# Optimization experiments

Hardware: AMD Instinct MI355X
Metric: run time of the kernel (lower is better)

Reference implementation:

```python
import jax, jax.numpy as jnp
import numpy as np

B, N, F_IN, F_OUT = 16, 1024, 128, 128
LEAKY_SLOPE = 0.01  # torch nn.LeakyReLU default


def setup_inputs() -> dict:
    key = jax.random.key(0)
    k1, k2, k3, k4 = jax.random.split(key, 4)
    node_mat = jax.random.normal(k1, (B, N, F_IN), dtype=jnp.float32)
    adj_mat = jax.random.uniform(k2, (B, N, N), dtype=jnp.float32)
    # nn.Linear(node_in_len, node_out_len): weight [F_OUT, F_IN], bias [F_OUT]
    bound = 1.0 / np.sqrt(F_IN)
    W = jax.random.uniform(k3, (F_OUT, F_IN), minval=-bound, maxval=bound, dtype=jnp.float32)
    b = jax.random.uniform(k4, (F_OUT,), minval=-bound, maxval=bound, dtype=jnp.float32)
    return {"node_mat": node_mat, "adj_mat": adj_mat, "W": W, "b": b}


def reference(node_mat, adj_mat, W, b):
    # degree normalization: row-scale adjacency by 1/degree
    # (the torch code builds a diagonal inv-degree matrix and bmm's it;
    #  mathematically identical to a broadcast row scale)
    n_neighbors = adj_mat.sum(axis=-1, keepdims=True)          # [B, N, 1]
    norm_adj = adj_mat / n_neighbors                           # [B, N, N]
    node_fea = jnp.einsum('bnm,bmf->bnf', norm_adj, node_mat)  # [B, N, F_in]
    node_fea = jnp.einsum('bnf,of->bno', node_fea, W) + b      # linear
    return jnp.where(node_fea >= 0, node_fea, LEAKY_SLOPE * node_fea)
```

## Files before the change

### kernel.cpp

```cpp
#include <hip/hip_runtime.h>
#include <hip/hip_bf16.h>


typedef __attribute__((ext_vector_type(8))) __bf16 bf16x8;
typedef __attribute__((ext_vector_type(4))) float f32x4;

#define GLD16(gp, lp) __builtin_amdgcn_global_load_lds( \
    (const __attribute__((address_space(1))) unsigned int*)(gp), \
    (__attribute__((address_space(3))) unsigned int*)(lp), 16, 0, 0)

#define WAITV8()  do { asm volatile("s_waitcnt vmcnt(8)" ::: "memory"); \
                       __builtin_amdgcn_sched_barrier(0); } while (0)
#define WAITV0()  do { asm volatile("s_waitcnt vmcnt(0)" ::: "memory"); \
                       __builtin_amdgcn_sched_barrier(0); } while (0)
#define BARF()    do { __builtin_amdgcn_s_barrier(); \
                       __builtin_amdgcn_sched_barrier(0); } while (0)

__device__ __forceinline__ unsigned f2bf_pk(float lo, float hi) {
    union { float f; unsigned u; } a, b;
    a.f = lo; b.f = hi;
    unsigned ra = (a.u + 0x7FFFu + ((a.u >> 16) & 1u)) >> 16;
    unsigned rb = (b.u + 0x7FFFu + ((b.u >> 16) & 1u)) & 0xFFFF0000u;
    return ra | rb;
}

__device__ __forceinline__ bf16x8 cvt8(const f32x4& a, const f32x4& b) {
    union { unsigned u[4]; bf16x8 v; } r;
    r.u[0] = f2bf_pk(a.x, a.y);
    r.u[1] = f2bf_pk(a.z, a.w);
    r.u[2] = f2bf_pk(b.x, b.y);
    r.u[3] = f2bf_pk(b.z, b.w);
    return r.v;
}

__global__ __launch_bounds__(256, 4)
void k1_xw(const float* __restrict__ x, const float* __restrict__ W,
           unsigned short* __restrict__ yF)
{
    __shared__ unsigned short Ax[16 * 128];
    __shared__ unsigned short Bw[128 * 128];

    const int t  = threadIdx.x;
    const int wg = blockIdx.x;
    const int b  = wg >> 6;
    const int m0 = (wg & 63) << 4;
    const float* xb = x + (((long)b << 10) + m0) * 128;

#pragma unroll
    for (int i = 0; i < 2; ++i) {
        int e = i * 1024 + t * 4;
        int r = e >> 7, f = e & 127;
        f32x4 v = *(const f32x4*)(xb + (long)r * 128 + f);
        int c = f >> 3;
        int byte = r * 256 + (((c ^ (r & 7)) << 4) | ((f & 7) << 1));
        uint2 pk; pk.x = f2bf_pk(v.x, v.y); pk.y = f2bf_pk(v.z, v.w);
        *(uint2*)((char*)Ax + byte) = pk;
    }
#pragma unroll
    for (int i = 0; i < 16; ++i) {
        int e = i * 1024 + t * 4;
        int r = e >> 7, f = e & 127;
        f32x4 v = *(const f32x4*)(W + r * 128 + f);
        int c = f >> 3;
        int byte = r * 256 + (((c ^ (r & 7)) << 4) | ((f & 7) << 1));
        uint2 pk; pk.x = f2bf_pk(v.x, v.y); pk.y = f2bf_pk(v.z, v.w);
        *(uint2*)((char*)Bw + byte) = pk;
    }
    __syncthreads();

    const int lane = t & 63, w = t >> 6;
    const int lrow = lane & 15, lq = lane >> 4;

    bf16x8 af[4];
#pragma unroll
    for (int kk = 0; kk < 4; ++kk) {
        int r = lrow;
        int c = kk * 4 + lq;
        af[kk] = *(const bf16x8*)((const char*)Ax + r * 256 + ((c ^ (r & 7)) << 4));
    }

    f32x4 zero = {0.f, 0.f, 0.f, 0.f};
    f32x4 acc[2] = {zero, zero};
#pragma unroll
    for (int nf = 0; nf < 2; ++nf) {
#pragma unroll
        for (int kk = 0; kk < 4; ++kk) {
            int o = (w * 2 + nf) * 16 + lrow;
            int c = kk * 4 + lq;
            bf16x8 bfrag = *(const bf16x8*)((const char*)Bw + o * 256 + ((c ^ (o & 7)) << 4));
            acc[nf] = __builtin_amdgcn_mfma_f32_16x16x32_bf16(af[kk], bfrag, acc[nf], 0, 0, 0);
        }
    }

    {
        const int ks = m0 >> 5;
        const int q  = ((m0 >> 4) & 1) * 2 + (lq >> 1);
        const int jb = (lq & 1) * 4;
#pragma unroll
        for (int nf = 0; nf < 2; ++nf) {
            int ot = w * 2 + nf;
            uint2 pk;
            pk.x = f2bf_pk(acc[nf][0], acc[nf][1]);
            pk.y = f2bf_pk(acc[nf][2], acc[nf][3]);
            long off = (((long)((b * 32 + ks) * 8 + ot)) << 9) + (q * 16 + lrow) * 8 + jb;
            *(uint2*)(yF + off) = pk;
        }
    }
}

__global__ __launch_bounds__(512, 1)
void k2_agg(const float* __restrict__ adj, const unsigned short* __restrict__ yF,
            const float* __restrict__ bias, float* __restrict__ out)
{
    __shared__ float          bufA[2][64 * 128];
    __shared__ unsigned short bufY[2][32 * 512];

    const int bid = blockIdx.x;
    const int xcd = bid & 7;
    const int j   = bid >> 3;
    const int b   = xcd * 2 + (j >> 4);
    const int n0  = (j & 15) << 6;

    const int t = threadIdx.x;
    const int lane = t & 63, w = t >> 6;
    const int h = w >> 1, oc = w & 1;
    const int lrow = lane & 15, lq = lane >> 4;

    const float* adjb = adj + ((long)b << 20);
    const int srow = (lane >> 5);
    const int ssc  = lane & 31;

    const float* ag[4];
    int adst[4];
#pragma unroll
    for (int i = 0; i < 4; ++i) {
        int rl = w * 8 + 2 * i + srow;
        ag[i]   = adjb + ((long)(n0 + rl) << 10) + ((ssc ^ (rl & 7)) << 2);
        adst[i] = (w * 8 + 2 * i) * 128;
    }
    const unsigned short* yg[4];
    int ydst[4];
#pragma unroll
    for (int i = 0; i < 4; ++i) {
        int f = w * 4 + i;
        yg[i]   = yF + (((long)((b * 32 + (f >> 3)) * 8 + (f & 7))) << 9) + lane * 8;
        ydst[i] = f << 9;
    }

    f32x4 zero = {0.f, 0.f, 0.f, 0.f};
    f32x4 acc[4] = {zero, zero, zero, zero};
    float dsum = 0.f;

#define STAGE(BUF, S)                                                   \
    do {                                                                \
        _Pragma("unroll")                                               \
        for (int i = 0; i < 4; ++i)                                     \
            GLD16(ag[i] + (S) * 128, &bufA[BUF][adst[i]]);              \
        _Pragma("unroll")                                               \
        for (int i = 0; i < 4; ++i)                                     \
            GLD16(yg[i] + (long)(S) * 16384, &bufY[BUF][ydst[i]]);      \
    } while (0)

    const int row = h * 16 + lrow;
    const int rx  = row & 7;

    STAGE(0, 0);
    int cur = 0;
#pragma unroll 2
    for (int s = 0; s < 8; ++s) {
        if (s < 7) {
            STAGE(cur ^ 1, s + 1);
            WAITV8();
        } else {
            WAITV0();
        }
        BARF();
#pragma unroll
        for (int kk = 0; kk < 4; ++kk) {
            const int c0 = kk * 8 + lq * 2;
            f32x4 a0 = *(const f32x4*)&bufA[cur][row * 128 + ((c0 ^ rx) << 2)];
            f32x4 a1 = *(const f32x4*)&bufA[cur][row * 128 + (((c0 + 1) ^ rx) << 2)];
            dsum += a0.x + a0.y + a0.z + a0.w + a1.x + a1.y + a1.z + a1.w;
            bf16x8 a = cvt8(a0, a1);
#pragma unroll
            for (int n = 0; n < 4; ++n) {
                const int ot = oc * 4 + n;
                bf16x8 bb = *(const bf16x8*)&bufY[cur][((kk * 8 + ot) << 9) + lane * 8];
                acc[n] = __builtin_amdgcn_mfma_f32_16x16x32_bf16(a, bb, acc[n], 0, 0, 0);
            }
        }
        BARF();
        cur ^= 1;
    }
#undef STAGE

    dsum += __shfl_xor(dsum, 16, 64);
    dsum += __shfl_xor(dsum, 32, 64);
    float invd[4];
#pragma unroll
    for (int i = 0; i < 4; ++i)
        invd[i] = 1.0f / __shfl(dsum, lq * 4 + i, 64);

#pragma unroll
    for (int n = 0; n < 4; ++n) {
        const int o = (oc * 4 + n) * 16 + lrow;
        const float bv = bias[o];
#pragma unroll
        for (int i = 0; i < 4; ++i) {
            const int r = n0 + h * 16 + lq * 4 + i;
            float v = acc[n][i] * invd[i] + bv;
            v = (v >= 0.f) ? v : 0.01f * v;
            out[(((long)(b * 1024 + r)) << 7) + o] = v;
        }
    }
}

extern "C" void kernel_launch(void* const* d_in, const int* in_sizes, int n_in,
                              void* d_out, int out_size, void* d_ws, size_t ws_size,
                              hipStream_t stream) {
    const float* node = (const float*)d_in[0];
    const float* adj  = (const float*)d_in[1];
    const float* W    = (const float*)d_in[2];
    const float* bias = (const float*)d_in[3];
    float* out = (float*)d_out;
    unsigned short* yF = (unsigned short*)d_ws;

    k1_xw<<<dim3(1024), dim3(256), 0, stream>>>(node, W, yF);
    k2_agg<<<dim3(256), dim3(512), 0, stream>>>(adj, yF, bias, out);
}
```

Measured before the change: 30.40 us.

## Pre-pack W into MFMA fragment layout once instead of per-block LDS staging

Adds a small kernel that converts W to bf16 in MFMA B-fragment order in workspace, so each k1 block reads its weight fragments directly from global memory instead of loading, converting and staging the full 128x128 W in LDS. The x tile is now copied with asynchronous global-to-LDS loads in fp32 and converted to bf16 at fragment read time. This removes the redundant per-block W conversion and the large LDS footprint, at the cost of an extra kernel launch and global-memory (cache) reads of W fragments.

```diff
diff --git a/kernel.cpp b/kernel.cpp
--- a/kernel.cpp
+++ b/kernel.cpp
@@ -34,61 +34,65 @@
 }
 
 __global__ __launch_bounds__(256, 4)
-void k1_xw(const float* __restrict__ x, const float* __restrict__ W,
+void k0_wf(const float* __restrict__ W, unsigned short* __restrict__ Wf)
+{
+    const int g   = blockIdx.x * 256 + threadIdx.x;
+    const int o   = g >> 4, fo = g & 15;
+    const int kk  = fo >> 2, sub = fo & 3;
+    const int l   = sub * 16 + (o & 15);
+    const int ot  = o >> 4;
+    const float* p = W + o * 128 + kk * 32 + sub * 8;
+    f32x4 v0 = *(const f32x4*)p;
+    f32x4 v1 = *(const f32x4*)(p + 4);
+    bf16x8 r = cvt8(v0, v1);
+    *(bf16x8*)(Wf + (((ot * 4 + kk) * 64 + l) << 3)) = r;
+}
+
+__global__ __launch_bounds__(256, 4)
+void k1_xw(const float* __restrict__ x, const unsigned short* __restrict__ Wf,
            unsigned short* __restrict__ yF)
 {
-    __shared__ unsigned short Ax[16 * 128];
-    __shared__ unsigned short Bw[128 * 128];
+    __shared__ float bufX[16 * 128];
 
     const int t  = threadIdx.x;
     const int wg = blockIdx.x;
     const int b  = wg >> 6;
     const int m0 = (wg & 63) << 4;
-    const float* xb = x + (((long)b << 10) + m0) * 128;
-
-#pragma unroll
-    for (int i = 0; i < 2; ++i) {
-        int e = i * 1024 + t * 4;
-        int r = e >> 7, f = e & 127;
-        f32x4 v = *(const f32x4*)(xb + (long)r * 128 + f);
-        int c = f >> 3;
-        int byte = r * 256 + (((c ^ (r & 7)) << 4) | ((f & 7) << 1));
-        uint2 pk; pk.x = f2bf_pk(v.x, v.y); pk.y = f2bf_pk(v.z, v.w);
-        *(uint2*)((char*)Ax + byte) = pk;
-    }
-#pragma unroll
-    for (int i = 0; i < 16; ++i) {
-        int e = i * 1024 + t * 4;
-        int r = e >> 7, f = e & 127;
-        f32x4 v = *(const f32x4*)(W + r * 128 + f);
-        int c = f >> 3;
-        int byte = r * 256 + (((c ^ (r & 7)) << 4) | ((f & 7) << 1));
-        uint2 pk; pk.x = f2bf_pk(v.x, v.y); pk.y = f2bf_pk(v.z, v.w);
-        *(uint2*)((char*)Bw + byte) = pk;
-    }
-    __syncthreads();
 
     const int lane = t & 63, w = t >> 6;
     const int lrow = lane & 15, lq = lane >> 4;
+    const int srow = lane >> 5;
+    const int ssc  = lane & 31;
+
+    const float* xb = x + (((long)b << 10) + m0) * 128;
+#pragma unroll
+    for (int i = 0; i < 2; ++i) {
+        int rl = w * 4 + 2 * i + srow;
+        const float* g = xb + ((long)rl << 7) + ((ssc ^ (rl & 7)) << 2);
+        GLD16(g, &bufX[(w * 4 + 2 * i) * 128]);
+    }
+    asm volatile("s_waitcnt vmcnt(0)" ::: "memory");
+    __syncthreads();
 
     bf16x8 af[4];
+    const int rx = lrow & 7;
 #pragma unroll
     for (int kk = 0; kk < 4; ++kk) {
-        int r = lrow;
-        int c = kk * 4 + lq;
-        af[kk] = *(const bf16x8*)((const char*)Ax + r * 256 + ((c ^ (r & 7)) << 4));
+        const int c0 = kk * 8 + lq * 2;
+        f32x4 a0 = *(const f32x4*)&bufX[lrow * 128 + ((c0 ^ rx) << 2)];
+        f32x4 a1 = *(const f32x4*)&bufX[lrow * 128 + (((c0 + 1) ^ rx) << 2)];
+        af[kk] = cvt8(a0, a1);
     }
 
     f32x4 zero = {0.f, 0.f, 0.f, 0.f};
     f32x4 acc[2] = {zero, zero};
 #pragma unroll
     for (int nf = 0; nf < 2; ++nf) {
+        const int ot = w * 2 + nf;
 #pragma unroll
         for (int kk = 0; kk < 4; ++kk) {
-            int o = (w * 2 + nf) * 16 + lrow;
-            int c = kk * 4 + lq;
-            bf16x8 bfrag = *(const bf16x8*)((const char*)Bw + o * 256 + ((c ^ (o & 7)) << 4));
-            acc[nf] = __builtin_amdgcn_mfma_f32_16x16x32_bf16(af[kk], bfrag, acc[nf], 0, 0, 0);
+            bf16x8 bw = *(const bf16x8*)(Wf + (((ot * 4 + kk) * 64 + lane) << 3));
+            acc[nf] = __builtin_amdgcn_mfma_f32_16x16x32_bf16(af[kk], bw, acc[nf], 0, 0, 0);
         }
     }
 
@@ -224,7 +228,9 @@
     const float* bias = (const float*)d_in[3];
     float* out = (float*)d_out;
     unsigned short* yF = (unsigned short*)d_ws;
-
-    k1_xw<<<dim3(1024), dim3(256), 0, stream>>>(node, W, yF);
+    unsigned short* Wf = (unsigned short*)((char*)d_ws + (4 << 20));
+
+    k0_wf<<<dim3(8), dim3(256), 0, stream>>>(W, Wf);
+    k1_xw<<<dim3(1024), dim3(256), 0, stream>>>(node, Wf, yF);
     k2_agg<<<dim3(256), dim3(512), 0, stream>>>(adj, yF, bias, out);
 }
```

Result: slower. 33.17 us (+9.1%).
